# Kernel tuning notes

Measured on AMD Instinct MI355X. Metric: run time of the kernel, lower is better.

Reference implementation:

```python
import jax, jax.numpy as jnp
import numpy as np

K = 3           # kernel_size
PAD = (K - 1) // 2
GC = 16         # group_channels (hardcoded in module)
EPS = 1e-5      # BatchNorm eps


def _extract_patches(x):
    # x: [B,C,H,W] -> [B,C,K*K,H,W], patch index = kh*K+kw (torch Unfold order)
    B, C, H, W = x.shape
    xp = jnp.pad(x, ((0, 0), (0, 0), (PAD, PAD), (PAD, PAD)))
    slices = [xp[:, :, i:i + H, j:j + W] for i in range(K) for j in range(K)]
    return jnp.stack(slices, axis=2)


def setup_inputs() -> dict:
    key = jax.random.key(0)
    ks = jax.random.split(key, 6)
    B, C, H, W = 4, 256, 128, 128
    Cr = C // 4                 # reduction_ratio = 4
    G = C // GC                 # groups = 16
    x = jax.random.normal(ks[0], (B, C, H, W), dtype=jnp.float32)
    # conv1: 1x1, C -> C/4, bias-free (followed by BN) + ReLU
    w1 = jax.random.normal(ks[1], (Cr, C), dtype=jnp.float32) * (1.0 / np.sqrt(C))
    bn_gamma = jnp.ones((Cr,), jnp.float32)
    bn_beta = jnp.zeros((Cr,), jnp.float32)
    bn_mean = jax.random.normal(ks[2], (Cr,), dtype=jnp.float32) * 0.1
    bn_var = jax.random.uniform(ks[3], (Cr,), dtype=jnp.float32, minval=0.5, maxval=1.5)
    # conv2: 1x1, C/4 -> K*K*groups, with bias, no norm/act
    w2 = jax.random.normal(ks[4], (K * K * G, Cr), dtype=jnp.float32) * (1.0 / np.sqrt(Cr))
    b2 = jax.random.normal(ks[5], (K * K * G,), dtype=jnp.float32) * 0.01
    return {"x": x, "w1": w1, "bn_gamma": bn_gamma, "bn_beta": bn_beta,
            "bn_mean": bn_mean, "bn_var": bn_var, "w2": w2, "b2": b2}


def reference(x, w1, bn_gamma, bn_beta, bn_mean, bn_var, w2, b2):
    B, C, H, W = x.shape
    G = C // GC
    # conv1 (1x1) + BN (inference) + ReLU
    h1 = jnp.einsum('bchw,oc->bohw', x, w1)
    inv_std = jax.lax.rsqrt(bn_var + EPS)
    h1 = (h1 - bn_mean[None, :, None, None]) * (bn_gamma * inv_std)[None, :, None, None] \
         + bn_beta[None, :, None, None]
    h1 = jax.nn.relu(h1)
    # conv2 (1x1) -> per-pixel dynamic kernels [B, G, K*K, H, W]
    wk = jnp.einsum('bchw,oc->bohw', h1, w2) + b2[None, :, None, None]
    wk = wk.reshape(B, G, K * K, H, W)
    # unfold x -> [B, G, GC, K*K, H, W], multiply by kernels and reduce over K*K
    patches = _extract_patches(x).reshape(B, G, GC, K * K, H, W)
    out = jnp.einsum('bgkhw,bgckhw->bgchw', wk, patches)
    return out.reshape(B, C, H, W)
```

## Files before the change

### kernel.cpp

```cpp
#include <hip/hip_runtime.h>

#define B_   4
#define C_   256
#define CR_  64
#define H_   128
#define W_   128
#define HW_  (H_ * W_)
#define G_   16
#define GC_  16
#define KO_  144
#define EPS_ 1e-5f

typedef __bf16 bf16x8 __attribute__((ext_vector_type(8)));
typedef __bf16 bf16x4 __attribute__((ext_vector_type(4)));
typedef __bf16 bf16x2 __attribute__((ext_vector_type(2)));
typedef float  f32x4  __attribute__((ext_vector_type(4)));

#define SX 66

__global__ void prep_kernel(const float* __restrict__ w1,
                            const float* __restrict__ gamma,
                            const float* __restrict__ beta,
                            const float* __restrict__ mean,
                            const float* __restrict__ var,
                            const float* __restrict__ w2,
                            __bf16* __restrict__ w1frag,
                            __bf16* __restrict__ w2frag,
                            float* __restrict__ bias2) {
    int idx = blockIdx.x * 256 + threadIdx.x;
    if (idx < 16384) {
        int kc = idx >> 11, r = idx & 2047;
        int mt = r >> 9, l = (r >> 3) & 63, j = r & 7;
        int o = mt * 16 + (l & 15);
        int c = kc * 32 + 8 * (l >> 4) + j;
        float alpha = gamma[o] * rsqrtf(var[o] + EPS_);
        w1frag[idx] = (__bf16)(w1[o * C_ + c] * alpha);
        if (idx < CR_) {
            float a2 = gamma[idx] * rsqrtf(var[idx] + EPS_);
            bias2[idx] = beta[idx] - mean[idx] * a2;
        }
    } else if (idx < 16384 + 9216) {
        int i2 = idx - 16384;
        int mt = i2 >> 10, r = i2 & 1023;
        int kc2 = r >> 9, l = (r >> 3) & 63, j = r & 7;
        int o2 = mt * 16 + (l & 15);
        int cc = kc2 * 32 + 8 * (l >> 4) + j;
        w2frag[i2] = (__bf16)(w2[o2 * CR_ + cc]);
    }
}

__global__ __launch_bounds__(256, 4) void conv12_kernel(
        const float* __restrict__ x,
        const __bf16* __restrict__ w1frag,
        const float* __restrict__ bias2,
        const __bf16* __restrict__ w2frag,
        const float* __restrict__ b2,
        __bf16* __restrict__ wk) {
    __shared__ __bf16 xs[2 * 32 * SX];
    __shared__ __bf16 hbuf[CR_ * SX];

    const int tid  = threadIdx.x;
    const int lane = tid & 63;
    const int wave = tid >> 6;
    const int wm = wave >> 1, wn = wave & 1;
    const int g = lane >> 4, n = lane & 15;

    const int bid = (blockIdx.x & 7) * 128 + (blockIdx.x >> 3);
    const int px0 = bid * 64;
    const int b   = px0 >> 14;
    const int hw0 = px0 & (HW_ - 1);

    const float* xb = x + (size_t)b * C_ * HW_ + hw0;
    const int krow = tid >> 3;
    const int t8   = tid & 7;

    {
        float4 v0 = *(const float4*)&xb[(size_t)krow * HW_ + 4 * t8];
        float4 v1 = *(const float4*)&xb[(size_t)krow * HW_ + 32 + 4 * t8];
        __bf16* d0 = &xs[krow * SX + 4 * t8];
        __bf16* d1 = &xs[krow * SX + 32 + 4 * t8];
        *(bf16x2*)&d0[0] = bf16x2{(__bf16)v0.x, (__bf16)v0.y};
        *(bf16x2*)&d0[2] = bf16x2{(__bf16)v0.z, (__bf16)v0.w};
        *(bf16x2*)&d1[0] = bf16x2{(__bf16)v1.x, (__bf16)v1.y};
        *(bf16x2*)&d1[2] = bf16x2{(__bf16)v1.z, (__bf16)v1.w};
    }
    __syncthreads();

    f32x4 acc1[2][2];
#pragma unroll
    for (int m = 0; m < 2; ++m)
#pragma unroll
        for (int t = 0; t < 2; ++t) acc1[m][t] = f32x4{0.f, 0.f, 0.f, 0.f};

    for (int kc = 0; kc < 8; ++kc) {
        const int buf = kc & 1;
        float4 nf0, nf1;
        if (kc < 7) {
            nf0 = *(const float4*)&xb[(size_t)(32 * (kc + 1) + krow) * HW_ + 4 * t8];
            nf1 = *(const float4*)&xb[(size_t)(32 * (kc + 1) + krow) * HW_ + 32 + 4 * t8];
        }
        bf16x8 a0 = *(const bf16x8*)&w1frag[((kc * 4 + 2 * wm + 0) * 64 + lane) * 8];
        bf16x8 a1 = *(const bf16x8*)&w1frag[((kc * 4 + 2 * wm + 1) * 64 + lane) * 8];
        const int base = buf * (32 * SX);
        bf16x8 b0, b1;
#pragma unroll
        for (int j = 0; j < 8; ++j) {
            b0[j] = xs[base + (8 * g + j) * SX + (2 * wn + 0) * 16 + n];
            b1[j] = xs[base + (8 * g + j) * SX + (2 * wn + 1) * 16 + n];
        }
        acc1[0][0] = __builtin_amdgcn_mfma_f32_16x16x32_bf16(a0, b0, acc1[0][0], 0, 0, 0);
        acc1[0][1] = __builtin_amdgcn_mfma_f32_16x16x32_bf16(a0, b1, acc1[0][1], 0, 0, 0);
        acc1[1][0] = __builtin_amdgcn_mfma_f32_16x16x32_bf16(a1, b0, acc1[1][0], 0, 0, 0);
        acc1[1][1] = __builtin_amdgcn_mfma_f32_16x16x32_bf16(a1, b1, acc1[1][1], 0, 0, 0);

        if (kc < 7) {
            __bf16* d0 = &xs[(buf ^ 1) * (32 * SX) + krow * SX + 4 * t8];
            __bf16* d1 = &xs[(buf ^ 1) * (32 * SX) + krow * SX + 32 + 4 * t8];
            *(bf16x2*)&d0[0] = bf16x2{(__bf16)nf0.x, (__bf16)nf0.y};
            *(bf16x2*)&d0[2] = bf16x2{(__bf16)nf0.z, (__bf16)nf0.w};
            *(bf16x2*)&d1[0] = bf16x2{(__bf16)nf1.x, (__bf16)nf1.y};
            *(bf16x2*)&d1[2] = bf16x2{(__bf16)nf1.z, (__bf16)nf1.w};
        }
        __syncthreads();
    }

#pragma unroll
    for (int m = 0; m < 2; ++m) {
        const int Mo = (2 * wm + m) * 16 + 4 * g;
        float4 bv = *(const float4*)&bias2[Mo];
        float bj[4] = {bv.x, bv.y, bv.z, bv.w};
#pragma unroll
        for (int t = 0; t < 2; ++t) {
            const int px = (2 * wn + t) * 16 + n;
#pragma unroll
            for (int j = 0; j < 4; ++j) {
                hbuf[(Mo + j) * SX + px] = (__bf16)fmaxf(acc1[m][t][j] + bj[j], 0.f);
            }
        }
    }
    __syncthreads();

    f32x4 acc2[9];
#pragma unroll
    for (int m = 0; m < 9; ++m) acc2[m] = f32x4{0.f, 0.f, 0.f, 0.f};

#pragma unroll
    for (int kc2 = 0; kc2 < 2; ++kc2) {
        bf16x8 hb;
#pragma unroll
        for (int j = 0; j < 8; ++j)
            hb[j] = hbuf[(kc2 * 32 + 8 * g + j) * SX + wave * 16 + n];
#pragma unroll
        for (int mt = 0; mt < 9; ++mt) {
            bf16x8 a = *(const bf16x8*)&w2frag[((mt * 2 + kc2) * 64 + lane) * 8];
            acc2[mt] = __builtin_amdgcn_mfma_f32_16x16x32_bf16(a, hb, acc2[mt], 0, 0, 0);
        }
    }

    __bf16* wkb = wk + (size_t)b * KO_ * HW_ + hw0 + wave * 16 + n;
#pragma unroll
    for (int mt = 0; mt < 9; ++mt) {
        const int o0 = mt * 16 + 4 * g;
        float4 bv = *(const float4*)&b2[o0];
        float bj[4] = {bv.x, bv.y, bv.z, bv.w};
#pragma unroll
        for (int j = 0; j < 4; ++j)
            wkb[(size_t)(o0 + j) * HW_] = (__bf16)(acc2[mt][j] + bj[j]);
    }
}

__global__ __launch_bounds__(256, 6) void inv_kernel(const float* __restrict__ x,
                                                     const __bf16* __restrict__ wkb,
                                                     float* __restrict__ out) {
    __shared__ __bf16 lds[96 * 128];
    const int bi   = (blockIdx.x & 7) * 256 + (blockIdx.x >> 3);
    const int tile = bi & 31;
    const int g    = (bi >> 5) & 15;
    const int b    = bi >> 9;
    const int h0   = tile * 4;
    const int tid  = threadIdx.x;
    const int lane = tid & 63;

    const float* xg = x + ((size_t)b * C_ + g * GC_) * HW_;
#pragma unroll
    for (int i = 0; i < 12; ++i) {
        int s = tid + 256 * i;
        int chrow = s >> 5, f4 = s & 31;
        int ch = chrow / 6, row = chrow - 6 * ch;
        int gh = h0 - 1 + row;
        float4 v = {0.f, 0.f, 0.f, 0.f};
        if (gh >= 0 && gh < H_)
            v = *(const float4*)&xg[((size_t)ch * H_ + gh) * W_ + f4 * 4];
        *(bf16x4*)&lds[chrow * 128 + f4 * 4] =
            bf16x4{(__bf16)v.x, (__bf16)v.y, (__bf16)v.z, (__bf16)v.w};
    }
    __syncthreads();

    const int q    = tid & 31;
    const int row  = (tid >> 5) & 3;
    const int half = tid >> 7;
    const int w0   = q * 4;
    const int hh   = h0 + row;
    const bool ql  = (q == 0);
    const bool qr  = (q == 31);

    float4 wk4[9];
    const __bf16* wkp = wkb + ((size_t)b * KO_ + g * 9) * HW_ + hh * W_ + w0;
#pragma unroll
    for (int k = 0; k < 9; ++k) {
        bf16x4 v = *(const bf16x4*)&wkp[(size_t)k * HW_];
        wk4[k] = float4{(float)v[0], (float)v[1], (float)v[2], (float)v[3]};
    }

    float* op = out + ((size_t)b * C_ + g * GC_ + half * 8) * HW_ + hh * W_ + w0;

#pragma unroll
    for (int cc = 0; cc < 8; ++cc) {
        const int ch = half * 8 + cc;
        const __bf16* base = &lds[(ch * 6 + row) * 128 + w0];
        float4 acc = {0.f, 0.f, 0.f, 0.f};
#pragma unroll
        for (int dr = 0; dr < 3; ++dr) {
            bf16x4 cv = *(const bf16x4*)(base + dr * 128);
            float4 c = {(float)cv[0], (float)cv[1], (float)cv[2], (float)cv[3]};
            float lms = __shfl(c.w, lane - 1);
            float rms = __shfl(c.x, lane + 1);
            float lm = ql ? 0.f : lms;
            float rm = qr ? 0.f : rms;
            float4 t0 = wk4[3 * dr + 0];
            float4 t1 = wk4[3 * dr + 1];
            float4 t2 = wk4[3 * dr + 2];
            acc.x = fmaf(t0.x, lm,  acc.x);
            acc.y = fmaf(t0.y, c.x, acc.y);
            acc.z = fmaf(t0.z, c.y, acc.z);
            acc.w = fmaf(t0.w, c.z, acc.w);
            acc.x = fmaf(t1.x, c.x, acc.x);
            acc.y = fmaf(t1.y, c.y, acc.y);
            acc.z = fmaf(t1.z, c.z, acc.z);
            acc.w = fmaf(t1.w, c.w, acc.w);
            acc.x = fmaf(t2.x, c.y, acc.x);
            acc.y = fmaf(t2.y, c.z, acc.y);
            acc.z = fmaf(t2.z, c.w, acc.z);
            acc.w = fmaf(t2.w, rm,  acc.w);
        }
        f32x4 av = {acc.x, acc.y, acc.z, acc.w};
        __builtin_nontemporal_store(av, (f32x4*)&op[(size_t)cc * HW_]);
    }
}

extern "C" void kernel_launch(void* const* d_in, const int* in_sizes, int n_in,
                              void* d_out, int out_size, void* d_ws, size_t ws_size,
                              hipStream_t stream) {
    const float* x     = (const float*)d_in[0];
    const float* w1    = (const float*)d_in[1];
    const float* gamma = (const float*)d_in[2];
    const float* beta  = (const float*)d_in[3];
    const float* mean  = (const float*)d_in[4];
    const float* var   = (const float*)d_in[5];
    const float* w2    = (const float*)d_in[6];
    const float* b2    = (const float*)d_in[7];
    float* out = (float*)d_out;

    char* ws = (char*)d_ws;
    __bf16* w1frag = (__bf16*)(ws);
    __bf16* w2frag = (__bf16*)(ws + (32 << 10));
    float*  bias2  = (float*)(ws + (56 << 10));
    __bf16* wkbuf  = (__bf16*)(ws + (1 << 20));

    hipLaunchKernelGGL(prep_kernel, dim3(100), dim3(256), 0, stream,
                       w1, gamma, beta, mean, var, w2, w1frag, w2frag, bias2);
    hipLaunchKernelGGL(conv12_kernel, dim3(1024), dim3(256), 0, stream,
                       x, w1frag, bias2, w2frag, b2, wkbuf);
    hipLaunchKernelGGL(inv_kernel, dim3(2048), dim3(256), 0, stream,
                       x, wkbuf, out);
}
```

Before: 51.52 us.

## Fuse kernel-generation convs and involution into one row-per-block kernel

```diff
diff --git a/kernel.cpp b/kernel.cpp
--- a/kernel.cpp
+++ b/kernel.cpp
@@ -13,10 +13,10 @@
 
 typedef __bf16 bf16x8 __attribute__((ext_vector_type(8)));
 typedef __bf16 bf16x4 __attribute__((ext_vector_type(4)));
-typedef __bf16 bf16x2 __attribute__((ext_vector_type(2)));
 typedef float  f32x4  __attribute__((ext_vector_type(4)));
 
-#define SX 66
+#define SX2 132
+#define WKS 132
 
 __global__ void prep_kernel(const float* __restrict__ w1,
                             const float* __restrict__ gamma,
@@ -49,15 +49,18 @@
     }
 }
 
-__global__ __launch_bounds__(256, 4) void conv12_kernel(
+__global__ __launch_bounds__(256, 2) void fused_kernel(
         const float* __restrict__ x,
         const __bf16* __restrict__ w1frag,
         const float* __restrict__ bias2,
         const __bf16* __restrict__ w2frag,
         const float* __restrict__ b2,
-        __bf16* __restrict__ wk) {
-    __shared__ __bf16 xs[2 * 32 * SX];
-    __shared__ __bf16 hbuf[CR_ * SX];
+        float* __restrict__ out) {
+    __shared__ __align__(16) char smem[71808];
+    __bf16* xs    = (__bf16*)smem;
+    __bf16* hbuf  = (__bf16*)(smem + 16896);
+    __bf16* wkbuf = (__bf16*)(smem + 33792);
+    __bf16* cbuf  = (__bf16*)smem;
 
     const int tid  = threadIdx.x;
     const int lane = tid & 63;
@@ -65,61 +68,62 @@
     const int wm = wave >> 1, wn = wave & 1;
     const int g = lane >> 4, n = lane & 15;
 
-    const int bid = (blockIdx.x & 7) * 128 + (blockIdx.x >> 3);
-    const int px0 = bid * 64;
-    const int b   = px0 >> 14;
-    const int hw0 = px0 & (HW_ - 1);
-
-    const float* xb = x + (size_t)b * C_ * HW_ + hw0;
-    const int krow = tid >> 3;
-    const int t8   = tid & 7;
-
-    {
-        float4 v0 = *(const float4*)&xb[(size_t)krow * HW_ + 4 * t8];
-        float4 v1 = *(const float4*)&xb[(size_t)krow * HW_ + 32 + 4 * t8];
-        __bf16* d0 = &xs[krow * SX + 4 * t8];
-        __bf16* d1 = &xs[krow * SX + 32 + 4 * t8];
-        *(bf16x2*)&d0[0] = bf16x2{(__bf16)v0.x, (__bf16)v0.y};
-        *(bf16x2*)&d0[2] = bf16x2{(__bf16)v0.z, (__bf16)v0.w};
-        *(bf16x2*)&d1[0] = bf16x2{(__bf16)v1.x, (__bf16)v1.y};
-        *(bf16x2*)&d1[2] = bf16x2{(__bf16)v1.z, (__bf16)v1.w};
+    const int bid = (blockIdx.x & 7) * 64 + (blockIdx.x >> 3);
+    const int b   = bid >> 7;
+    const int h   = bid & 127;
+
+    const float* xrow = x + (size_t)b * C_ * HW_ + h * W_;
+
+#pragma unroll
+    for (int i = 0; i < 4; ++i) {
+        int s = tid + 256 * i;
+        int cl = s >> 5, f4i = s & 31;
+        float4 v = *(const float4*)&xrow[(size_t)cl * HW_ + f4i * 4];
+        *(bf16x4*)&xs[cl * SX2 + f4i * 4] =
+            bf16x4{(__bf16)v.x, (__bf16)v.y, (__bf16)v.z, (__bf16)v.w};
     }
     __syncthreads();
 
-    f32x4 acc1[2][2];
+    f32x4 acc1[2][4];
 #pragma unroll
     for (int m = 0; m < 2; ++m)
 #pragma unroll
-        for (int t = 0; t < 2; ++t) acc1[m][t] = f32x4{0.f, 0.f, 0.f, 0.f};
+        for (int t = 0; t < 4; ++t) acc1[m][t] = f32x4{0.f, 0.f, 0.f, 0.f};
 
     for (int kc = 0; kc < 8; ++kc) {
         const int buf = kc & 1;
-        float4 nf0, nf1;
+        float4 nf[4];
         if (kc < 7) {
-            nf0 = *(const float4*)&xb[(size_t)(32 * (kc + 1) + krow) * HW_ + 4 * t8];
-            nf1 = *(const float4*)&xb[(size_t)(32 * (kc + 1) + krow) * HW_ + 32 + 4 * t8];
+#pragma unroll
+            for (int i = 0; i < 4; ++i) {
+                int s = tid + 256 * i;
+                int cl = s >> 5, f4i = s & 31;
+                nf[i] = *(const float4*)&xrow[(size_t)(32 * (kc + 1) + cl) * HW_ + f4i * 4];
+            }
         }
         bf16x8 a0 = *(const bf16x8*)&w1frag[((kc * 4 + 2 * wm + 0) * 64 + lane) * 8];
         bf16x8 a1 = *(const bf16x8*)&w1frag[((kc * 4 + 2 * wm + 1) * 64 + lane) * 8];
-        const int base = buf * (32 * SX);
-        bf16x8 b0, b1;
-#pragma unroll
-        for (int j = 0; j < 8; ++j) {
-            b0[j] = xs[base + (8 * g + j) * SX + (2 * wn + 0) * 16 + n];
-            b1[j] = xs[base + (8 * g + j) * SX + (2 * wn + 1) * 16 + n];
-        }
-        acc1[0][0] = __builtin_amdgcn_mfma_f32_16x16x32_bf16(a0, b0, acc1[0][0], 0, 0, 0);
-        acc1[0][1] = __builtin_amdgcn_mfma_f32_16x16x32_bf16(a0, b1, acc1[0][1], 0, 0, 0);
-        acc1[1][0] = __builtin_amdgcn_mfma_f32_16x16x32_bf16(a1, b0, acc1[1][0], 0, 0, 0);
-        acc1[1][1] = __builtin_amdgcn_mfma_f32_16x16x32_bf16(a1, b1, acc1[1][1], 0, 0, 0);
-
+        const int base = buf * (32 * SX2);
+        bf16x8 bt[4];
+#pragma unroll
+        for (int t = 0; t < 4; ++t)
+#pragma unroll
+            for (int j = 0; j < 8; ++j)
+                bt[t][j] = xs[base + (8 * g + j) * SX2 + (4 * wn + t) * 16 + n];
+#pragma unroll
+        for (int t = 0; t < 4; ++t) {
+            acc1[0][t] = __builtin_amdgcn_mfma_f32_16x16x32_bf16(a0, bt[t], acc1[0][t], 0, 0, 0);
+            acc1[1][t] = __builtin_amdgcn_mfma_f32_16x16x32_bf16(a1, bt[t], acc1[1][t], 0, 0, 0);
+        }
         if (kc < 7) {
-            __bf16* d0 = &xs[(buf ^ 1) * (32 * SX) + krow * SX + 4 * t8];
-            __bf16* d1 = &xs[(buf ^ 1) * (32 * SX) + krow * SX + 32 + 4 * t8];
-            *(bf16x2*)&d0[0] = bf16x2{(__bf16)nf0.x, (__bf16)nf0.y};
-            *(bf16x2*)&d0[2] = bf16x2{(__bf16)nf0.z, (__bf16)nf0.w};
-            *(bf16x2*)&d1[0] = bf16x2{(__bf16)nf1.x, (__bf16)nf1.y};
-            *(bf16x2*)&d1[2] = bf16x2{(__bf16)nf1.z, (__bf16)nf1.w};
+            const int nb = (buf ^ 1) * (32 * SX2);
+#pragma unroll
+            for (int i = 0; i < 4; ++i) {
+                int s = tid + 256 * i;
+                int cl = s >> 5, f4i = s & 31;
+                *(bf16x4*)&xs[nb + cl * SX2 + f4i * 4] =
+                    bf16x4{(__bf16)nf[i].x, (__bf16)nf[i].y, (__bf16)nf[i].z, (__bf16)nf[i].w};
+            }
         }
         __syncthreads();
     }
@@ -130,121 +134,115 @@
         float4 bv = *(const float4*)&bias2[Mo];
         float bj[4] = {bv.x, bv.y, bv.z, bv.w};
 #pragma unroll
-        for (int t = 0; t < 2; ++t) {
-            const int px = (2 * wn + t) * 16 + n;
-#pragma unroll
-            for (int j = 0; j < 4; ++j) {
-                hbuf[(Mo + j) * SX + px] = (__bf16)fmaxf(acc1[m][t][j] + bj[j], 0.f);
-            }
+        for (int t = 0; t < 4; ++t) {
+            const int px = (4 * wn + t) * 16 + n;
+#pragma unroll
+            for (int j = 0; j < 4; ++j)
+                hbuf[(Mo + j) * SX2 + px] = (__bf16)fmaxf(acc1[m][t][j] + bj[j], 0.f);
         }
     }
     __syncthreads();
 
-    f32x4 acc2[9];
-#pragma unroll
-    for (int m = 0; m < 9; ++m) acc2[m] = f32x4{0.f, 0.f, 0.f, 0.f};
+    f32x4 acc2[9][2];
+#pragma unroll
+    for (int m = 0; m < 9; ++m)
+#pragma unroll
+        for (int t = 0; t < 2; ++t) acc2[m][t] = f32x4{0.f, 0.f, 0.f, 0.f};
 
 #pragma unroll
     for (int kc2 = 0; kc2 < 2; ++kc2) {
-        bf16x8 hb;
-#pragma unroll
-        for (int j = 0; j < 8; ++j)
-            hb[j] = hbuf[(kc2 * 32 + 8 * g + j) * SX + wave * 16 + n];
+        bf16x8 hb[2];
+#pragma unroll
+        for (int t2 = 0; t2 < 2; ++t2)
+#pragma unroll
+            for (int j = 0; j < 8; ++j)
+                hb[t2][j] = hbuf[(kc2 * 32 + 8 * g + j) * SX2 + (2 * wave + t2) * 16 + n];
 #pragma unroll
         for (int mt = 0; mt < 9; ++mt) {
             bf16x8 a = *(const bf16x8*)&w2frag[((mt * 2 + kc2) * 64 + lane) * 8];
-            acc2[mt] = __builtin_amdgcn_mfma_f32_16x16x32_bf16(a, hb, acc2[mt], 0, 0, 0);
-        }
-    }
-
-    __bf16* wkb = wk + (size_t)b * KO_ * HW_ + hw0 + wave * 16 + n;
+            acc2[mt][0] = __builtin_amdgcn_mfma_f32_16x16x32_bf16(a, hb[0], acc2[mt][0], 0, 0, 0);
+            acc2[mt][1] = __builtin_amdgcn_mfma_f32_16x16x32_bf16(a, hb[1], acc2[mt][1], 0, 0, 0);
+        }
+    }
+
 #pragma unroll
     for (int mt = 0; mt < 9; ++mt) {
         const int o0 = mt * 16 + 4 * g;
         float4 bv = *(const float4*)&b2[o0];
         float bj[4] = {bv.x, bv.y, bv.z, bv.w};
 #pragma unroll
-        for (int j = 0; j < 4; ++j)
-            wkb[(size_t)(o0 + j) * HW_] = (__bf16)(acc2[mt][j] + bj[j]);
-    }
-}
-
-__global__ __launch_bounds__(256, 6) void inv_kernel(const float* __restrict__ x,
-                                                     const __bf16* __restrict__ wkb,
-                                                     float* __restrict__ out) {
-    __shared__ __bf16 lds[96 * 128];
-    const int bi   = (blockIdx.x & 7) * 256 + (blockIdx.x >> 3);
-    const int tile = bi & 31;
-    const int g    = (bi >> 5) & 15;
-    const int b    = bi >> 9;
-    const int h0   = tile * 4;
-    const int tid  = threadIdx.x;
-    const int lane = tid & 63;
-
-    const float* xg = x + ((size_t)b * C_ + g * GC_) * HW_;
-#pragma unroll
-    for (int i = 0; i < 12; ++i) {
-        int s = tid + 256 * i;
-        int chrow = s >> 5, f4 = s & 31;
-        int ch = chrow / 6, row = chrow - 6 * ch;
-        int gh = h0 - 1 + row;
-        float4 v = {0.f, 0.f, 0.f, 0.f};
-        if (gh >= 0 && gh < H_)
-            v = *(const float4*)&xg[((size_t)ch * H_ + gh) * W_ + f4 * 4];
-        *(bf16x4*)&lds[chrow * 128 + f4 * 4] =
-            bf16x4{(__bf16)v.x, (__bf16)v.y, (__bf16)v.z, (__bf16)v.w};
+        for (int t2 = 0; t2 < 2; ++t2) {
+            const int px = (2 * wave + t2) * 16 + n;
+#pragma unroll
+            for (int j = 0; j < 4; ++j)
+                wkbuf[(o0 + j) * WKS + px] = (__bf16)(acc2[mt][t2][j] + bj[j]);
+        }
     }
     __syncthreads();
 
-    const int q    = tid & 31;
-    const int row  = (tid >> 5) & 3;
-    const int half = tid >> 7;
-    const int w0   = q * 4;
-    const int hh   = h0 + row;
-    const bool ql  = (q == 0);
-    const bool qr  = (q == 31);
-
-    float4 wk4[9];
-    const __bf16* wkp = wkb + ((size_t)b * KO_ + g * 9) * HW_ + hh * W_ + w0;
-#pragma unroll
-    for (int k = 0; k < 9; ++k) {
-        bf16x4 v = *(const bf16x4*)&wkp[(size_t)k * HW_];
-        wk4[k] = float4{(float)v[0], (float)v[1], (float)v[2], (float)v[3]};
-    }
-
-    float* op = out + ((size_t)b * C_ + g * GC_ + half * 8) * HW_ + hh * W_ + w0;
-
-#pragma unroll
-    for (int cc = 0; cc < 8; ++cc) {
-        const int ch = half * 8 + cc;
-        const __bf16* base = &lds[(ch * 6 + row) * 128 + w0];
-        float4 acc = {0.f, 0.f, 0.f, 0.f};
-#pragma unroll
-        for (int dr = 0; dr < 3; ++dr) {
-            bf16x4 cv = *(const bf16x4*)(base + dr * 128);
-            float4 c = {(float)cv[0], (float)cv[1], (float)cv[2], (float)cv[3]};
-            float lms = __shfl(c.w, lane - 1);
-            float rms = __shfl(c.x, lane + 1);
-            float lm = ql ? 0.f : lms;
-            float rm = qr ? 0.f : rms;
-            float4 t0 = wk4[3 * dr + 0];
-            float4 t1 = wk4[3 * dr + 1];
-            float4 t2 = wk4[3 * dr + 2];
-            acc.x = fmaf(t0.x, lm,  acc.x);
-            acc.y = fmaf(t0.y, c.x, acc.y);
-            acc.z = fmaf(t0.z, c.y, acc.z);
-            acc.w = fmaf(t0.w, c.z, acc.w);
-            acc.x = fmaf(t1.x, c.x, acc.x);
-            acc.y = fmaf(t1.y, c.y, acc.y);
-            acc.z = fmaf(t1.z, c.z, acc.z);
-            acc.w = fmaf(t1.w, c.w, acc.w);
-            acc.x = fmaf(t2.x, c.y, acc.x);
-            acc.y = fmaf(t2.y, c.z, acc.y);
-            acc.z = fmaf(t2.z, c.w, acc.z);
-            acc.w = fmaf(t2.w, rm,  acc.w);
-        }
-        f32x4 av = {acc.x, acc.y, acc.z, acc.w};
-        __builtin_nontemporal_store(av, (f32x4*)&op[(size_t)cc * HW_]);
+    const int q  = tid & 31;
+    const int cp = tid >> 5;
+    const int w0 = q * 4;
+    const bool ql = (q == 0), qr = (q == 31);
+
+    for (int chunk = 0; chunk < 8; ++chunk) {
+        const int ch0 = chunk * 32;
+#pragma unroll
+        for (int i = 0; i < 12; ++i) {
+            int s = tid + 256 * i;
+            int rr = s >> 5, f4i = s & 31;
+            int cl = rr / 3, r = rr - 3 * cl;
+            int gh = h - 1 + r;
+            float4 v = {0.f, 0.f, 0.f, 0.f};
+            if (gh >= 0 && gh < H_)
+                v = *(const float4*)&x[((size_t)(b * C_ + ch0 + cl)) * HW_ + gh * W_ + f4i * 4];
+            *(bf16x4*)&cbuf[rr * SX2 + f4i * 4] =
+                bf16x4{(__bf16)v.x, (__bf16)v.y, (__bf16)v.z, (__bf16)v.w};
+        }
+        __syncthreads();
+
+        const int gq = (ch0 + cp * 4) >> 4;
+        float4 wk4[9];
+#pragma unroll
+        for (int k = 0; k < 9; ++k) {
+            bf16x4 v = *(const bf16x4*)&wkbuf[(gq * 9 + k) * WKS + w0];
+            wk4[k] = float4{(float)v[0], (float)v[1], (float)v[2], (float)v[3]};
+        }
+
+#pragma unroll
+        for (int i2 = 0; i2 < 4; ++i2) {
+            const int cl = cp * 4 + i2;
+            const __bf16* bse = &cbuf[(cl * 3) * SX2 + w0];
+            float4 acc = {0.f, 0.f, 0.f, 0.f};
+#pragma unroll
+            for (int dr = 0; dr < 3; ++dr) {
+                bf16x4 cv = *(const bf16x4*)(bse + dr * SX2);
+                float4 c = {(float)cv[0], (float)cv[1], (float)cv[2], (float)cv[3]};
+                float lms = __shfl(c.w, lane - 1);
+                float rms = __shfl(c.x, lane + 1);
+                float lm = ql ? 0.f : lms;
+                float rm = qr ? 0.f : rms;
+                float4 t0 = wk4[3 * dr + 0];
+                float4 t1 = wk4[3 * dr + 1];
+                float4 t2 = wk4[3 * dr + 2];
+                acc.x = fmaf(t0.x, lm,  acc.x);
+                acc.y = fmaf(t0.y, c.x, acc.y);
+                acc.z = fmaf(t0.z, c.y, acc.z);
+                acc.w = fmaf(t0.w, c.z, acc.w);
+                acc.x = fmaf(t1.x, c.x, acc.x);
+                acc.y = fmaf(t1.y, c.y, acc.y);
+                acc.z = fmaf(t1.z, c.z, acc.z);
+                acc.w = fmaf(t1.w, c.w, acc.w);
+                acc.x = fmaf(t2.x, c.y, acc.x);
+                acc.y = fmaf(t2.y, c.z, acc.y);
+                acc.z = fmaf(t2.z, c.w, acc.z);
+                acc.w = fmaf(t2.w, rm,  acc.w);
+            }
+            f32x4 av = {acc.x, acc.y, acc.z, acc.w};
+            __builtin_nontemporal_store(av,
+                (f32x4*)&out[((size_t)(b * C_ + ch0 + cl)) * HW_ + h * W_ + w0]);
+        }
+        __syncthreads();
     }
 }
 
@@ -265,12 +263,9 @@
     __bf16* w1frag = (__bf16*)(ws);
     __bf16* w2frag = (__bf16*)(ws + (32 << 10));
     float*  bias2  = (float*)(ws + (56 << 10));
-    __bf16* wkbuf  = (__bf16*)(ws + (1 << 20));
 
     hipLaunchKernelGGL(prep_kernel, dim3(100), dim3(256), 0, stream,
                        w1, gamma, beta, mean, var, w2, w1frag, w2frag, bias2);
-    hipLaunchKernelGGL(conv12_kernel, dim3(1024), dim3(256), 0, stream,
-                       x, w1frag, bias2, w2frag, b2, wkbuf);
-    hipLaunchKernelGGL(inv_kernel, dim3(2048), dim3(256), 0, stream,
-                       x, wkbuf, out);
+    hipLaunchKernelGGL(fused_kernel, dim3(512), dim3(256), 0, stream,
+                       x, w1frag, bias2, w2frag, b2, out);
 }
```

Result: slower. 61.38 us, median of 2 (+19.1%).
